# Performance work log

Measured on AMD Instinct MI355X. Metric: run time of the kernel, lower is better.

The kernel has to match this reference:

```python
import jax, jax.numpy as jnp
import numpy as np

LEAKY_SLOPE = 0.05        # self.alpha is overwritten to 0.05 in __init__
NEG_INF = -9.0e15         # masking constant from the source
THRESH = 0.5              # connection_threshold

B, N, F = 8, 2048, 128


def setup_inputs() -> dict:
    key = jax.random.key(0)
    k1, k2, k3, k4, k5 = jax.random.split(key, 5)
    h = jax.random.normal(k1, (B, N, F), dtype=jnp.float32)
    W = jax.random.normal(k2, (F, F), dtype=jnp.float32) * (1.414 / np.sqrt(F))
    a = jax.random.normal(k3, (2 * F, 1), dtype=jnp.float32) * 0.1
    A1 = jax.random.normal(k4, (4 * N, N), dtype=jnp.float32) * (1.414 / np.sqrt(N))
    A2 = jax.random.normal(k5, (N, 4 * N), dtype=jnp.float32) * (1.414 / np.sqrt(4 * N))
    return {"h": h, "W": W, "a": a, "A1": A1, "A2": A2}


def reference(h, W, a, A1, A2):
    f = W.shape[0]
    # Wh = h @ W^T  (torch Linear stores weight as [out, in])
    Wh = jnp.einsum('bnf,gf->bng', h, W)                       # [B,N,F]
    # additive GAT scores: e[b,i,j] = leaky_relu(Wh_i.a1 + Wh_j.a2)
    Wh1 = Wh @ a[:f, :]                                        # [B,N,1]
    Wh2 = Wh @ a[f:, :]                                        # [B,N,1]
    e = Wh1 + jnp.swapaxes(Wh2, 1, 2)                          # [B,N,N]
    e = jnp.where(e > 0, e, LEAKY_SLOPE * e)                   # LeakyReLU(0.05)
    # learned adjacency gate over last dim (computed in the original forward
    # but never used for the returned output -> dead code; kept for fidelity)
    hid = jax.nn.sigmoid(jnp.einsum('bij,hj->bih', e, A1))     # [B,N,4N]
    adj = jax.nn.sigmoid(e + jnp.einsum('bih,jh->bij', hid, A2))
    adj = jnp.where(adj > THRESH, adj, 0.0)                    # unused downstream
    # masked softmax attention over e itself
    attention = jax.nn.softmax(jnp.where(e > 0, e, NEG_INF), axis=2)
    # dropout is identity in eval mode (training=False)
    h_prime = jnp.einsum('bij,bjf->bif', attention, Wh)        # [B,N,F]
    return jax.nn.elu(h_prime)                                 # concat=True branch
```

## Files before the change

### kernel.cpp

```cpp
#include <hip/hip_runtime.h>
#include <math.h>

#define BB 8
#define NN 2048
#define FF 128
#define CH 128
#define CHSZ 16

typedef __attribute__((ext_vector_type(8))) short short8;
typedef __attribute__((ext_vector_type(4))) float f32x4;

__device__ __forceinline__ ushort f2bf(float x) {
    uint u = __float_as_uint(x);
    uint r = (u + 0x7FFFu + ((u >> 16) & 1u)) >> 16;
    return (ushort)r;
}
__device__ __forceinline__ float bf2f(ushort x) {
    return __uint_as_float(((uint)x) << 16);
}

__global__ __launch_bounds__(256) void k1_wh(
        const float* __restrict__ h, const float* __restrict__ W,
        const float* __restrict__ a, float* __restrict__ Wh,
        float* __restrict__ s1, float* __restrict__ s2) {
    __shared__ __align__(16) ushort Whi[128][136];
    __shared__ __align__(16) ushort Wlo[128][136];
    __shared__ __align__(16) ushort hhi[64][136];
    __shared__ __align__(16) ushort hlo[64][136];
    const int tid = threadIdx.x;
    const int row0 = blockIdx.x * 64;

    for (int i = tid; i < 4096; i += 256) {
        int g = i >> 5, k4 = (i & 31) * 4;
        float4 wv = *(const float4*)&W[g * 128 + k4];
        ushort h0 = f2bf(wv.x), h1 = f2bf(wv.y), h2 = f2bf(wv.z), h3 = f2bf(wv.w);
        ushort l0 = f2bf(wv.x - bf2f(h0)), l1 = f2bf(wv.y - bf2f(h1));
        ushort l2 = f2bf(wv.z - bf2f(h2)), l3 = f2bf(wv.w - bf2f(h3));
        uint2 hw, lw;
        hw.x = (uint)h0 | ((uint)h1 << 16); hw.y = (uint)h2 | ((uint)h3 << 16);
        lw.x = (uint)l0 | ((uint)l1 << 16); lw.y = (uint)l2 | ((uint)l3 << 16);
        *(uint2*)&Whi[g][k4] = hw;
        *(uint2*)&Wlo[g][k4] = lw;
    }
    for (int i = tid; i < 2048; i += 256) {
        int r = i >> 5, k4 = (i & 31) * 4;
        float4 hv = *(const float4*)&h[(row0 + r) * 128 + k4];
        ushort h0 = f2bf(hv.x), h1 = f2bf(hv.y), h2 = f2bf(hv.z), h3 = f2bf(hv.w);
        ushort l0 = f2bf(hv.x - bf2f(h0)), l1 = f2bf(hv.y - bf2f(h1));
        ushort l2 = f2bf(hv.z - bf2f(h2)), l3 = f2bf(hv.w - bf2f(h3));
        uint2 hw, lw;
        hw.x = (uint)h0 | ((uint)h1 << 16); hw.y = (uint)h2 | ((uint)h3 << 16);
        lw.x = (uint)l0 | ((uint)l1 << 16); lw.y = (uint)l2 | ((uint)l3 << 16);
        *(uint2*)&hhi[r][k4] = hw;
        *(uint2*)&hlo[r][k4] = lw;
    }
    __syncthreads();

    const int lane = tid & 63;
    const int wid = tid >> 6;
    const int gl = lane & 15;
    const int kg = lane >> 4;
    const int lr = wid * 16 + gl;

    f32x4 acc[8];
#pragma unroll
    for (int gt = 0; gt < 8; ++gt) acc[gt] = (f32x4){0.f, 0.f, 0.f, 0.f};

#pragma unroll
    for (int t = 0; t < 4; ++t) {
        const int k0 = t * 32 + kg * 8;
        short8 ah = *(const short8*)&hhi[lr][k0];
        short8 al = *(const short8*)&hlo[lr][k0];
#pragma unroll
        for (int gt = 0; gt < 8; ++gt) {
            const int g = gt * 16 + gl;
            short8 bh = *(const short8*)&Whi[g][k0];
            short8 bl = *(const short8*)&Wlo[g][k0];
            acc[gt] = __builtin_amdgcn_mfma_f32_16x16x32_bf16(ah, bh, acc[gt], 0, 0, 0);
            acc[gt] = __builtin_amdgcn_mfma_f32_16x16x32_bf16(ah, bl, acc[gt], 0, 0, 0);
            acc[gt] = __builtin_amdgcn_mfma_f32_16x16x32_bf16(al, bh, acc[gt], 0, 0, 0);
        }
    }

    float p1a[4] = {0.f, 0.f, 0.f, 0.f}, p2a[4] = {0.f, 0.f, 0.f, 0.f};
#pragma unroll
    for (int gt = 0; gt < 8; ++gt) {
        const int g = gt * 16 + gl;
        const float a1v = a[g];
        const float a2v = a[128 + g];
#pragma unroll
        for (int r = 0; r < 4; ++r) {
            float wvv = acc[gt][r];
            Wh[(row0 + wid * 16 + kg * 4 + r) * 128 + g] = wvv;
            p1a[r] += wvv * a1v;
            p2a[r] += wvv * a2v;
        }
    }
#pragma unroll
    for (int s = 1; s < 16; s <<= 1) {
#pragma unroll
        for (int r = 0; r < 4; ++r) {
            p1a[r] += __shfl_xor(p1a[r], s, 64);
            p2a[r] += __shfl_xor(p2a[r], s, 64);
        }
    }
    if (gl == 0) {
#pragma unroll
        for (int r = 0; r < 4; ++r) {
            int row = row0 + wid * 16 + kg * 4 + r;
            s1[row] = p1a[r];
            s2[row] = p2a[r];
        }
    }
}

__global__ __launch_bounds__(512) void k2_rank(
        const float* __restrict__ s2, const float* __restrict__ s1,
        int* __restrict__ idxs, float* __restrict__ ps,
        int* __restrict__ lo_arr) {
    __shared__ __align__(16) float ls[NN];
    __shared__ int part[8][64];
    __shared__ int lpart[8][64];
    __shared__ float wmax[8];
    const int t = threadIdx.x;
    const int blk = blockIdx.x;
    const int b = blk >> 5;
    const int seg = blk & 31;
    const int base = b * NN;
    float4* ls4 = (float4*)ls;
    const float4* g4 = (const float4*)(s2 + base);
    float m;
    {
        float4 v4 = g4[t];
        ls4[t] = v4;
        m = fmaxf(fmaxf(v4.x, v4.y), fmaxf(v4.z, v4.w));
    }
#pragma unroll
    for (int s = 1; s < 64; s <<= 1) m = fmaxf(m, __shfl_xor(m, s, 64));
    if ((t & 63) == 0) wmax[t >> 6] = m;
    __syncthreads();
    float M = wmax[0];
#pragma unroll
    for (int i = 1; i < 8; ++i) M = fmaxf(M, wmax[i]);
    const int jj = t & 63;
    const int w  = t >> 6;
    const int j  = seg * 64 + jj;
    const float v = ls[j];
    const float s1v = s1[base + j];
    int rank = 0, cnt = 0;
#pragma unroll 8
    for (int q = 0; q < 64; ++q) {
        float4 kv = ls4[w * 64 + q];
        int kg = w * 256 + q * 4;
        rank += (kv.x < v) | ((kv.x == v) & (kg + 0 < j));
        rank += (kv.y < v) | ((kv.y == v) & (kg + 1 < j));
        rank += (kv.z < v) | ((kv.z == v) & (kg + 2 < j));
        rank += (kv.w < v) | ((kv.w == v) & (kg + 3 < j));
        cnt += (s1v + kv.x <= 0.f);
        cnt += (s1v + kv.y <= 0.f);
        cnt += (s1v + kv.z <= 0.f);
        cnt += (s1v + kv.w <= 0.f);
    }
    part[w][jj] = rank;
    lpart[w][jj] = cnt;
    __syncthreads();
    if (t < 64) {
        int r = 0, lo = 0;
#pragma unroll
        for (int ww = 0; ww < 8; ++ww) {
            r  += part[ww][t];
            lo += lpart[ww][t];
        }
        int jg = seg * 64 + t;
        float vv = ls[jg];
        idxs[base + r] = jg;
        ps[base + r] = expf(vv - M);
        lo_arr[base + jg] = lo;
    }
}

__global__ __launch_bounds__(128) void k3_scan(
        const float* __restrict__ Wh, const int* __restrict__ idxs,
        const float* __restrict__ ps,
        float* __restrict__ partial, float* __restrict__ psuf,
        float* __restrict__ chunktot, float* __restrict__ chunku,
        float* __restrict__ chunkp) {
    const int blk = blockIdx.x;
    const int b = blk >> 7, c = blk & 127;
    const int base = b * NN;
    const int f = threadIdx.x;
    float acc = 0.f, accu = 0.f, pacc = 0.f;
#pragma unroll
    for (int tt = CHSZ - 1; tt >= 0; --tt) {
        int r = c * CHSZ + tt;
        int jj = idxs[base + r];
        float pv = ps[base + r];
        float w = Wh[(base + jj) * 128 + f];
        acc += pv * w;
        accu += w;
        pacc += pv;
        partial[(base + r) * 128 + f] = acc;
        if (f == 0) psuf[base + r] = pacc;
    }
    chunktot[(b * CH + c) * 128 + f] = acc;
    chunku[(b * CH + c) * 128 + f] = accu;
    if (f == 0) chunkp[b * CH + c] = pacc;
}

__global__ __launch_bounds__(512) void k4_merged(
        const float* __restrict__ chunktot, const float* __restrict__ chunku,
        const float* __restrict__ chunkp,
        const int* __restrict__ lo_arr, const float* __restrict__ psuf,
        const float* __restrict__ partial, float* __restrict__ out) {
    __shared__ __align__(16) float cs[CH][132];
    __shared__ float segt[4][128];
    __shared__ float mvp[4][128];
    __shared__ float mv[128];
    __shared__ float lp[CH];
    const int tid = threadIdx.x;
    const int blk = blockIdx.x;
    const int b = blk >> 5;
    const int base = b * NN;
    const int f = tid & 127;
    const int q = tid >> 7;

    float suf[32];
    float acc = 0.f, su = 0.f;
#pragma unroll
    for (int i = 31; i >= 0; --i) {
        int c = q * 32 + i;
        acc += chunktot[(b * CH + c) * 128 + f];
        su  += chunku[(b * CH + c) * 128 + f];
        suf[i] = acc;
    }
    segt[q][f] = acc;
    mvp[q][f] = su;

    if (tid < 64) {
        float p0 = chunkp[b * CH + tid * 2];
        float p1v = chunkp[b * CH + tid * 2 + 1];
        float S = p0 + p1v;
        float T = S;
#pragma unroll
        for (int s = 1; s < 64; s <<= 1) {
            float t2 = __shfl_down(T, s, 64);
            if (tid + s < 64) T += t2;
        }
        float E = __shfl_down(T, 1, 64);
        if (tid == 63) E = 0.f;
        lp[tid * 2]     = p0 + p1v + E;
        lp[tid * 2 + 1] = p1v + E;
    }
    __syncthreads();

    float off = 0.f;
#pragma unroll
    for (int qq = 1; qq < 4; ++qq)
        if (q + qq < 4) off += segt[q + qq][f];
#pragma unroll
    for (int i = 0; i < 32; ++i)
        cs[q * 32 + i][f] = suf[i] + off;
    if (tid < 128)
        mv[tid] = (mvp[0][tid] + mvp[1][tid] + mvp[2][tid] + mvp[3][tid])
                  * (1.f / (float)NN);
    __syncthreads();

#pragma unroll
    for (int pass = 0; pass < 4; ++pass) {
        const int rowg = blk * 64 + pass * 16 + (tid >> 5);
        const int fq = (tid & 31) * 4;
        const int lo = lo_arr[rowg];
        float4 v;
        if (lo == NN) {
            v = make_float4(mv[fq], mv[fq + 1], mv[fq + 2], mv[fq + 3]);
        } else {
            const int c = lo >> 4;
            float4 pp = *(const float4*)&partial[(base + lo) * 128 + fq];
            float4 csv = make_float4(0.f, 0.f, 0.f, 0.f);
            float lps = 0.f;
            if (c < CH - 1) {
                csv = *(const float4*)&cs[c + 1][fq];
                lps = lp[c + 1];
            }
            float den = psuf[base + lo] + lps;
            v.x = (pp.x + csv.x) / den;
            v.y = (pp.y + csv.y) / den;
            v.z = (pp.z + csv.z) / den;
            v.w = (pp.w + csv.w) / den;
        }
        v.x = (v.x > 0.f) ? v.x : expm1f(v.x);
        v.y = (v.y > 0.f) ? v.y : expm1f(v.y);
        v.z = (v.z > 0.f) ? v.z : expm1f(v.z);
        v.w = (v.w > 0.f) ? v.w : expm1f(v.w);
        *(float4*)&out[rowg * 128 + fq] = v;
    }
}

extern "C" void kernel_launch(void* const* d_in, const int* in_sizes, int n_in,
                              void* d_out, int out_size, void* d_ws, size_t ws_size,
                              hipStream_t stream) {
    (void)in_sizes; (void)n_in; (void)out_size; (void)ws_size;
    const float* h = (const float*)d_in[0];
    const float* W = (const float*)d_in[1];
    const float* a = (const float*)d_in[2];
    float* out = (float*)d_out;

    float* Wh       = (float*)d_ws;
    float* partial  = Wh + 2097152;
    float* s1       = partial + 2097152;
    float* s2       = s1 + 16384;
    float* ps       = s2 + 16384;
    float* psuf     = ps + 16384;
    int*   idxs     = (int*)(psuf + 16384);
    int*   lo_arr   = idxs + 16384;
    float* chunktot = (float*)(lo_arr + 16384);
    float* chunku   = chunktot + 131072;
    float* chunkp   = chunku + 131072;

    k1_wh<<<BB * NN / 64, 256, 0, stream>>>(h, W, a, Wh, s1, s2);
    k2_rank<<<BB * 32, 512, 0, stream>>>(s2, s1, idxs, ps, lo_arr);
    k3_scan<<<BB * CH, 128, 0, stream>>>(Wh, idxs, ps, partial, psuf,
                                         chunktot, chunku, chunkp);
    k4_merged<<<BB * 32, 512, 0, stream>>>(chunktot, chunku, chunkp,
                                           lo_arr, psuf, partial, out);
}
```

Measured before the change: 170.0 us.

## Fuse chunk scan into output kernel and recompute per-row partial sums on the fly

```diff
diff --git a/kernel.cpp b/kernel.cpp
--- a/kernel.cpp
+++ b/kernel.cpp
@@ -179,68 +179,72 @@
     }
 }
 
-__global__ __launch_bounds__(128) void k3_scan(
+__global__ __launch_bounds__(512) void k34(
         const float* __restrict__ Wh, const int* __restrict__ idxs,
-        const float* __restrict__ ps,
-        float* __restrict__ partial, float* __restrict__ psuf,
-        float* __restrict__ chunktot, float* __restrict__ chunku,
-        float* __restrict__ chunkp) {
-    const int blk = blockIdx.x;
-    const int b = blk >> 7, c = blk & 127;
-    const int base = b * NN;
-    const int f = threadIdx.x;
-    float acc = 0.f, accu = 0.f, pacc = 0.f;
-#pragma unroll
-    for (int tt = CHSZ - 1; tt >= 0; --tt) {
-        int r = c * CHSZ + tt;
-        int jj = idxs[base + r];
-        float pv = ps[base + r];
-        float w = Wh[(base + jj) * 128 + f];
-        acc += pv * w;
-        accu += w;
-        pacc += pv;
-        partial[(base + r) * 128 + f] = acc;
-        if (f == 0) psuf[base + r] = pacc;
-    }
-    chunktot[(b * CH + c) * 128 + f] = acc;
-    chunku[(b * CH + c) * 128 + f] = accu;
-    if (f == 0) chunkp[b * CH + c] = pacc;
-}
-
-__global__ __launch_bounds__(512) void k4_merged(
-        const float* __restrict__ chunktot, const float* __restrict__ chunku,
-        const float* __restrict__ chunkp,
-        const int* __restrict__ lo_arr, const float* __restrict__ psuf,
-        const float* __restrict__ partial, float* __restrict__ out) {
+        const float* __restrict__ ps, const int* __restrict__ lo_arr,
+        float* __restrict__ out) {
     __shared__ __align__(16) float cs[CH][132];
+    __shared__ float lp[CH];
+    __shared__ float mvp[8][128];
+    __shared__ float mv[128];
     __shared__ float segt[4][128];
-    __shared__ float mvp[4][128];
-    __shared__ float mv[128];
-    __shared__ float lp[CH];
+    __shared__ __align__(16) int   lidx[NN];
+    __shared__ __align__(16) float lps[NN];
     const int tid = threadIdx.x;
     const int blk = blockIdx.x;
     const int b = blk >> 5;
     const int base = b * NN;
+
+    *(int4*)&lidx[tid * 4]  = ((const int4*)(idxs + base))[tid];
+    *(float4*)&lps[tid * 4] = ((const float4*)(ps + base))[tid];
+    __syncthreads();
+
+    {
+        const int lane = tid & 63;
+        const int w = tid >> 6;
+        const int f2 = lane * 2;
+        float ux = 0.f, uy = 0.f;
+#pragma unroll 2
+        for (int cc = 0; cc < 16; ++cc) {
+            const int c = w * 16 + cc;
+            float ax = 0.f, ay = 0.f, pacc = 0.f;
+#pragma unroll
+            for (int t = CHSZ - 1; t >= 0; --t) {
+                const int r = c * CHSZ + t;
+                const int j = lidx[r];
+                const float pv = lps[r];
+                float2 wv = *(const float2*)&Wh[(base + j) * 128 + f2];
+                ax += pv * wv.x;
+                ay += pv * wv.y;
+                ux += wv.x;
+                uy += wv.y;
+                pacc += pv;
+            }
+            cs[c][f2] = ax;
+            cs[c][f2 + 1] = ay;
+            if (lane == 0) lp[c] = pacc;
+        }
+        mvp[w][f2] = ux;
+        mvp[w][f2 + 1] = uy;
+    }
+    __syncthreads();
+
+    const int q = tid >> 7;
     const int f = tid & 127;
-    const int q = tid >> 7;
-
     float suf[32];
-    float acc = 0.f, su = 0.f;
-#pragma unroll
-    for (int i = 31; i >= 0; --i) {
-        int c = q * 32 + i;
-        acc += chunktot[(b * CH + c) * 128 + f];
-        su  += chunku[(b * CH + c) * 128 + f];
-        suf[i] = acc;
-    }
-    segt[q][f] = acc;
-    mvp[q][f] = su;
-
+    {
+        float acc = 0.f;
+#pragma unroll
+        for (int i = 31; i >= 0; --i) {
+            acc += cs[q * 32 + i][f];
+            suf[i] = acc;
+        }
+        segt[q][f] = acc;
+    }
     if (tid < 64) {
-        float p0 = chunkp[b * CH + tid * 2];
-        float p1v = chunkp[b * CH + tid * 2 + 1];
-        float S = p0 + p1v;
-        float T = S;
+        float p0 = lp[tid * 2];
+        float p1v = lp[tid * 2 + 1];
+        float T = p0 + p1v;
 #pragma unroll
         for (int s = 1; s < 64; s <<= 1) {
             float t2 = __shfl_down(T, s, 64);
@@ -251,18 +255,22 @@
         lp[tid * 2]     = p0 + p1v + E;
         lp[tid * 2 + 1] = p1v + E;
     }
-    __syncthreads();
-
-    float off = 0.f;
-#pragma unroll
-    for (int qq = 1; qq < 4; ++qq)
-        if (q + qq < 4) off += segt[q + qq][f];
-#pragma unroll
-    for (int i = 0; i < 32; ++i)
-        cs[q * 32 + i][f] = suf[i] + off;
-    if (tid < 128)
-        mv[tid] = (mvp[0][tid] + mvp[1][tid] + mvp[2][tid] + mvp[3][tid])
-                  * (1.f / (float)NN);
+    if (tid < 128) {
+        float s = 0.f;
+#pragma unroll
+        for (int ww = 0; ww < 8; ++ww) s += mvp[ww][tid];
+        mv[tid] = s * (1.f / (float)NN);
+    }
+    __syncthreads();
+    {
+        float off = 0.f;
+#pragma unroll
+        for (int qq = 1; qq < 4; ++qq)
+            if (q + qq < 4) off += segt[q + qq][f];
+#pragma unroll
+        for (int i = 0; i < 32; ++i)
+            cs[q * 32 + i][f] = suf[i] + off;
+    }
     __syncthreads();
 
 #pragma unroll
@@ -275,14 +283,25 @@
             v = make_float4(mv[fq], mv[fq + 1], mv[fq + 2], mv[fq + 3]);
         } else {
             const int c = lo >> 4;
-            float4 pp = *(const float4*)&partial[(base + lo) * 128 + fq];
+            float4 pp = make_float4(0.f, 0.f, 0.f, 0.f);
+            float den_p = 0.f;
+            for (int r = c * CHSZ + CHSZ - 1; r >= lo; --r) {
+                const int j = lidx[r];
+                const float pv = lps[r];
+                float4 wv = *(const float4*)&Wh[(base + j) * 128 + fq];
+                pp.x += pv * wv.x;
+                pp.y += pv * wv.y;
+                pp.z += pv * wv.z;
+                pp.w += pv * wv.w;
+                den_p += pv;
+            }
             float4 csv = make_float4(0.f, 0.f, 0.f, 0.f);
-            float lps = 0.f;
+            float lpE = 0.f;
             if (c < CH - 1) {
                 csv = *(const float4*)&cs[c + 1][fq];
-                lps = lp[c + 1];
+                lpE = lp[c + 1];
             }
-            float den = psuf[base + lo] + lps;
+            const float den = den_p + lpE;
             v.x = (pp.x + csv.x) / den;
             v.y = (pp.y + csv.y) / den;
             v.z = (pp.z + csv.z) / den;
@@ -305,22 +324,14 @@
     const float* a = (const float*)d_in[2];
     float* out = (float*)d_out;
 
-    float* Wh       = (float*)d_ws;
-    float* partial  = Wh + 2097152;
-    float* s1       = partial + 2097152;
-    float* s2       = s1 + 16384;
-    float* ps       = s2 + 16384;
-    float* psuf     = ps + 16384;
-    int*   idxs     = (int*)(psuf + 16384);
-    int*   lo_arr   = idxs + 16384;
-    float* chunktot = (float*)(lo_arr + 16384);
-    float* chunku   = chunktot + 131072;
-    float* chunkp   = chunku + 131072;
+    float* Wh     = (float*)d_ws;
+    float* s1     = Wh + 2097152;
+    float* s2     = s1 + 16384;
+    float* ps     = s2 + 16384;
+    int*   idxs   = (int*)(ps + 16384);
+    int*   lo_arr = idxs + 16384;
 
     k1_wh<<<BB * NN / 64, 256, 0, stream>>>(h, W, a, Wh, s1, s2);
     k2_rank<<<BB * 32, 512, 0, stream>>>(s2, s1, idxs, ps, lo_arr);
-    k3_scan<<<BB * CH, 128, 0, stream>>>(Wh, idxs, ps, partial, psuf,
-                                         chunktot, chunku, chunkp);
-    k4_merged<<<BB * 32, 512, 0, stream>>>(chunktot, chunku, chunkp,
-                                           lo_arr, psuf, partial, out);
-}
+    k34<<<BB * 32, 512, 0, stream>>>(Wh, idxs, ps, lo_arr, out);
+}
```

Measured after the change: 193.1 us. 1.14x slower.
